# Kernel tuning notes

Measured on AMD Instinct MI355X. Metric: run time of the kernel, lower is better.

Reference implementation:

```python
import jax, jax.numpy as jnp
import numpy as np

T, B, IN, H, L = 512, 64, 512, 512, 2
GATE = 4 * H


def setup_inputs() -> dict:
    key = jax.random.key(0)
    ks = jax.random.split(key, 8)
    s_in = 1.0 / np.sqrt(IN)
    s_h = 1.0 / np.sqrt(H)
    return {
        "x": jax.random.normal(ks[0], (T, B, IN), dtype=jnp.float32),
        # layer 0 params (nn.Linear stores weight as [out, in]; y = x @ W.T + b)
        "Wi0": jax.random.uniform(ks[1], (GATE, IN), jnp.float32, -s_in, s_in),
        "bi0": jax.random.uniform(ks[2], (GATE,), jnp.float32, -s_in, s_in),
        "Wh0": jax.random.uniform(ks[3], (GATE, H), jnp.float32, -s_h, s_h),
        # layer 1 params
        "Wi1": jax.random.uniform(ks[4], (GATE, H), jnp.float32, -s_h, s_h),
        "bi1": jax.random.uniform(ks[5], (GATE,), jnp.float32, -s_h, s_h),
        "Wh1": jax.random.uniform(ks[6], (GATE, H), jnp.float32, -s_h, s_h),
    }


def _run_layer(x_seq, Wi, bi, Wh):
    """Scan the subLSTM cell over time. x_seq: [T, B, in] -> [T, B, H]."""
    Bs = x_seq.shape[1]
    h0 = jnp.zeros((Bs, H), x_seq.dtype)
    c0 = jnp.zeros((Bs, H), x_seq.dtype)

    def cell(carry, x_t):
        h, c = carry
        # all four gates are sigmoid in subLSTM
        g = jax.nn.sigmoid(x_t @ Wi.T + bi + h @ Wh.T)  # [B, 4H]
        in_gate, out_gate, z_t, f_gate = jnp.split(g, 4, axis=-1)
        c_new = c * f_gate + z_t - in_gate          # subtractive combine
        h_new = jax.nn.sigmoid(c_new) - out_gate    # subtractive output
        return (h_new, c_new), h_new

    (_, _), out = jax.lax.scan(cell, (h0, c0), x_seq)
    return out


def reference(x, Wi0, bi0, Wh0, Wi1, bi1, Wh1):
    out = _run_layer(x, Wi0, bi0, Wh0)
    out = _run_layer(out, Wi1, bi1, Wh1)
    return out  # [T, B, H] (batch_first=False, dropout=0)
```

## Files before the change

### kernel.cpp

```cpp
#include <hip/hip_runtime.h>
#include <stdint.h>

#define TSTEPS 512
#define BATCH  64
#define HDIM   512
#define GATE   2048
#define ACTMAT (BATCH * HDIM)
#define SENT   0xFFFFFFFFu
#define NWORK  128

typedef __attribute__((ext_vector_type(8))) _Float16 f16x8;
typedef __attribute__((ext_vector_type(4))) float f32x4;
typedef __attribute__((ext_vector_type(4))) uint32_t u32x4;
typedef __attribute__((ext_vector_type(2))) uint32_t u32x2;

__device__ __forceinline__ unsigned short f2h(float f) {
  union { _Float16 h; unsigned short u; } v;
  v.h = (_Float16)f;
  return v.u;
}
__device__ __forceinline__ float fsigmoid(float x) {
  return 1.0f / (1.0f + __expf(-x));
}


__global__ void init_h(unsigned short* h0, unsigned short* h1) {
  size_t u = (size_t)blockIdx.x * blockDim.x + threadIdx.x;
  u32x4 v;
  if (u < (ACTMAT * 2 / 16)) v = (u32x4){0u, 0u, 0u, 0u};
  else                       v = (u32x4){SENT, SENT, SENT, SENT};
  ((u32x4*)h0)[u] = v;
  ((u32x4*)h1)[u] = v;
}

__global__ void convert_x(const float* __restrict__ x, unsigned short* __restrict__ xh) {
  size_t i = (size_t)(blockIdx.x * blockDim.x + threadIdx.x) * 4;
  float4 v = *(const float4*)(x + i);
  ushort4 o = make_ushort4(f2h(v.x), f2h(v.y), f2h(v.z), f2h(v.w));
  *(ushort4*)(xh + i) = o;
}

__global__ void split_w(const float* __restrict__ Wi, const float* __restrict__ Wh,
                        unsigned short* __restrict__ Wf) {
  int i = blockIdx.x * blockDim.x + threadIdx.x;
  int G = i >> 10, k = i & 1023;
  float w = (k < 512) ? Wi[((size_t)G << 9) + k] : Wh[((size_t)G << 9) + (k - 512)];
  Wf[i] = f2h(w);
}


__global__ __launch_bounds__(128, 1)
void sublstm_persistent(const unsigned short* __restrict__ xh,
                        unsigned short* h0, unsigned short* h1,
                        const unsigned short* __restrict__ Wf0,
                        const unsigned short* __restrict__ Wf1,
                        const float* __restrict__ bi0, const float* __restrict__ bi1,
                        float* __restrict__ out)
{
  __shared__ unsigned short wlds[64][1024];

  const int wg    = blockIdx.x;
  const int tid   = threadIdx.x;
  const int layer = wg >> 6;
  const int wgl   = wg & 63;
  const int s     = wgl & 31;
  const int p     = wgl >> 5;
  const int j0    = s << 4;
  const int b0    = p << 5;
  const int lane  = tid & 63;
  const int wr    = tid >> 6;

  const unsigned short* Wf = layer ? Wf1 : Wf0;
  const float* bi = layer ? bi1 : bi0;

  for (int idx = tid; idx < 8192; idx += 128) {
    int n = idx >> 7;
    int u = idx & 127;
    int G = ((n >> 4) << 9) + j0 + (n & 15);
    const unsigned short* sp = Wf + ((size_t)G << 10) + ((size_t)u << 3);
    *(uint4*)&wlds[n][(u ^ (n & 15)) << 3] = *(const uint4*)sp;
  }
  __syncthreads();

  const int c15 = lane & 15;
  const int g4  = lane >> 4;
  const int sw  = c15;
  const int brow = b0 + (wr << 4) + c15;
  const int jb   = j0 + (g4 << 2);
  const size_t arow = (size_t)brow * HDIM;
  const size_t hoff = arow + jb;

  const float4 bq0 = *(const float4*)&bi[jb];
  const float4 bq1 = *(const float4*)&bi[512 + jb];
  const float4 bq2 = *(const float4*)&bi[1024 + jb];
  const float4 bq3 = *(const float4*)&bi[1536 + jb];

  float cs0 = 0.0f, cs1 = 0.0f, cs2 = 0.0f, cs3 = 0.0f;

#define CONSUME(R, KK, UB) do {                                                        \
    f16x8 a = __builtin_bit_cast(f16x8, (R));                                          \
    int u_ = ((UB) + ((KK) << 2) + g4) ^ sw;                                           \
    f16x8 w0 = *(const f16x8*)&wlds[c15][u_ << 3];                                     \
    f16x8 w1 = *(const f16x8*)&wlds[16 + c15][u_ << 3];                                \
    f16x8 w2 = *(const f16x8*)&wlds[32 + c15][u_ << 3];                                \
    f16x8 w3 = *(const f16x8*)&wlds[48 + c15][u_ << 3];                                \
    acc0 = __builtin_amdgcn_mfma_f32_16x16x32_f16(w0, a, acc0, 0, 0, 0);               \
    acc1 = __builtin_amdgcn_mfma_f32_16x16x32_f16(w1, a, acc1, 0, 0, 0);               \
    acc2 = __builtin_amdgcn_mfma_f32_16x16x32_f16(w2, a, acc2, 0, 0, 0);               \
    acc3 = __builtin_amdgcn_mfma_f32_16x16x32_f16(w3, a, acc3, 0, 0, 0);               \
  } while (0)

#define CONSUME_ALL(P, UB)                                                             \
    CONSUME(P##0, 0, UB);  CONSUME(P##1, 1, UB);  CONSUME(P##2, 2, UB);                \
    CONSUME(P##3, 3, UB);  CONSUME(P##4, 4, UB);  CONSUME(P##5, 5, UB);                \
    CONSUME(P##6, 6, UB);  CONSUME(P##7, 7, UB);  CONSUME(P##8, 8, UB);                \
    CONSUME(P##9, 9, UB);  CONSUME(P##10, 10, UB); CONSUME(P##11, 11, UB);             \
    CONSUME(P##12, 12, UB); CONSUME(P##13, 13, UB); CONSUME(P##14, 14, UB);            \
    CONSUME(P##15, 15, UB)

#define LD1(R, OFFTOK, HP)                                                             \
    asm volatile("global_load_dwordx4 %0, %1, off " OFFTOK " sc0 sc1"                  \
                 : "=v"(R) : "v"(HP) : "memory")

#define ISSUE16(HP, P) do {                                                            \
    LD1(P##0, "", HP);            LD1(P##1, "offset:64", HP);                          \
    LD1(P##2, "offset:128", HP);  LD1(P##3, "offset:192", HP);                         \
    LD1(P##4, "offset:256", HP);  LD1(P##5, "offset:320", HP);                         \
    LD1(P##6, "offset:384", HP);  LD1(P##7, "offset:448", HP);                         \
    LD1(P##8, "offset:512", HP);  LD1(P##9, "offset:576", HP);                         \
    LD1(P##10, "offset:640", HP); LD1(P##11, "offset:704", HP);                        \
    LD1(P##12, "offset:768", HP); LD1(P##13, "offset:832", HP);                        \
    LD1(P##14, "offset:896", HP); LD1(P##15, "offset:960", HP);                        \
  } while (0)

#define BAD1(R) ((R[0] == SENT) | (R[1] == SENT) | (R[2] == SENT) | (R[3] == SENT))

#define VALIDATE(HP, P) do {                                                           \
    for (;;) {                                                                         \
      asm volatile("s_waitcnt vmcnt(0)" ::: "memory");                                 \
      __builtin_amdgcn_sched_barrier(0);                                               \
      int bad_ = BAD1(P##0) | BAD1(P##1) | BAD1(P##2) | BAD1(P##3) |                   \
                 BAD1(P##4) | BAD1(P##5) | BAD1(P##6) | BAD1(P##7) |                   \
                 BAD1(P##8) | BAD1(P##9) | BAD1(P##10) | BAD1(P##11) |                 \
                 BAD1(P##12) | BAD1(P##13) | BAD1(P##14) | BAD1(P##15);                \
      if (!__any(bad_)) break;                                                         \
      ISSUE16(HP, P);                                                                  \
    }                                                                                  \
    __builtin_amdgcn_sched_barrier(0);                                                 \
  } while (0)

#define KHALF_X(AP) do {                                                               \
    const unsigned short* ap_ = (AP) + arow + (g4 << 3);                               \
    _Pragma("unroll")                                                                  \
    for (int kk = 0; kk < 16; ++kk) {                                                  \
      u32x4 rr = *(const u32x4*)(ap_ + (kk << 5));                                     \
      CONSUME(rr, kk, 0);                                                              \
    }                                                                                  \
  } while (0)

#define EPILOGUE(T) do {                                                               \
    unsigned short* hn = (layer ? h1 : h0) + (size_t)((T) + 1) * ACTMAT;               \
    float gi_, go_, gz_, gf_, h0v, h1v, h2v, h3v;                                      \
    gi_ = fsigmoid(acc0[0] + bq0.x); go_ = fsigmoid(acc1[0] + bq1.x);                  \
    gz_ = fsigmoid(acc2[0] + bq2.x); gf_ = fsigmoid(acc3[0] + bq3.x);                  \
    cs0 = cs0 * gf_ + gz_ - gi_;  h0v = fsigmoid(cs0) - go_;                           \
    gi_ = fsigmoid(acc0[1] + bq0.y); go_ = fsigmoid(acc1[1] + bq1.y);                  \
    gz_ = fsigmoid(acc2[1] + bq2.y); gf_ = fsigmoid(acc3[1] + bq3.y);                  \
    cs1 = cs1 * gf_ + gz_ - gi_;  h1v = fsigmoid(cs1) - go_;                           \
    gi_ = fsigmoid(acc0[2] + bq0.z); go_ = fsigmoid(acc1[2] + bq1.z);                  \
    gz_ = fsigmoid(acc2[2] + bq2.z); gf_ = fsigmoid(acc3[2] + bq3.z);                  \
    cs2 = cs2 * gf_ + gz_ - gi_;  h2v = fsigmoid(cs2) - go_;                           \
    gi_ = fsigmoid(acc0[3] + bq0.w); go_ = fsigmoid(acc1[3] + bq1.w);                  \
    gz_ = fsigmoid(acc2[3] + bq2.w); gf_ = fsigmoid(acc3[3] + bq3.w);                  \
    cs3 = cs3 * gf_ + gz_ - gi_;  h3v = fsigmoid(cs3) - go_;                           \
    u32x2 dv;                                                                          \
    dv[0] = (uint32_t)f2h(h0v) | ((uint32_t)f2h(h1v) << 16);                           \
    dv[1] = (uint32_t)f2h(h2v) | ((uint32_t)f2h(h3v) << 16);                           \
    asm volatile("global_store_dwordx2 %0, %1, off sc0 sc1"                            \
                 :: "v"((uint32_t*)(hn + hoff)), "v"(dv) : "memory");                  \
    if (layer) {                                                                       \
      float* outp = out + (size_t)(T) * ACTMAT;                                        \
      *(float4*)(outp + hoff) = make_float4(h0v, h1v, h2v, h3v);                       \
    }                                                                                  \
  } while (0)

  if (layer == 0) {
    for (int t = 0; t < TSTEPS; ++t) {
      f32x4 acc0 = {}, acc1 = {}, acc2 = {}, acc3 = {};
      u32x4 ra0, ra1, ra2, ra3, ra4, ra5, ra6, ra7,
            ra8, ra9, ra10, ra11, ra12, ra13, ra14, ra15;
      const unsigned short* hp = h0 + (size_t)t * ACTMAT + arow + (g4 << 3);
      ISSUE16(hp, ra);
      KHALF_X(xh + (size_t)t * ACTMAT);
      VALIDATE(hp, ra);
      CONSUME_ALL(ra, 64);
      EPILOGUE(t);
    }
  } else {
    for (int t = 0; t < TSTEPS; ++t) {
      f32x4 acc0 = {}, acc1 = {}, acc2 = {}, acc3 = {};
      u32x4 ra0, ra1, ra2, ra3, ra4, ra5, ra6, ra7,
            ra8, ra9, ra10, ra11, ra12, ra13, ra14, ra15;
      u32x4 rb0, rb1, rb2, rb3, rb4, rb5, rb6, rb7,
            rb8, rb9, rb10, rb11, rb12, rb13, rb14, rb15;
      const unsigned short* hpA = h1 + (size_t)t * ACTMAT + arow + (g4 << 3);
      const unsigned short* hpB = h0 + (size_t)(t + 1) * ACTMAT + arow + (g4 << 3);
      ISSUE16(hpA, ra);
      ISSUE16(hpB, rb);
      VALIDATE(hpA, ra);
      CONSUME_ALL(ra, 64);
      VALIDATE(hpB, rb);
      CONSUME_ALL(rb, 0);
      EPILOGUE(t);
    }
  }
#undef CONSUME
#undef CONSUME_ALL
#undef LD1
#undef ISSUE16
#undef BAD1
#undef VALIDATE
#undef KHALF_X
#undef EPILOGUE
}


extern "C" void kernel_launch(void* const* d_in, const int* in_sizes, int n_in,
                              void* d_out, int out_size, void* d_ws, size_t ws_size,
                              hipStream_t stream) {
  (void)in_sizes; (void)n_in; (void)out_size; (void)ws_size;
  const float* x   = (const float*)d_in[0];
  const float* Wi0 = (const float*)d_in[1];
  const float* bi0 = (const float*)d_in[2];
  const float* Wh0 = (const float*)d_in[3];
  const float* Wi1 = (const float*)d_in[4];
  const float* bi1 = (const float*)d_in[5];
  const float* Wh1 = (const float*)d_in[6];
  float* out = (float*)d_out;

  char* ws = (char*)d_ws;
  size_t off = 0;
  auto take = [&](size_t bytes) -> void* {
    void* p = ws + off;
    off += (bytes + 255) & ~(size_t)255;
    return p;
  };
  unsigned short* xh  = (unsigned short*)take((size_t)TSTEPS * ACTMAT * 2);
  unsigned short* h0  = (unsigned short*)take((size_t)(TSTEPS + 1) * ACTMAT * 2);
  unsigned short* h1  = (unsigned short*)take((size_t)(TSTEPS + 1) * ACTMAT * 2);
  unsigned short* Wf0 = (unsigned short*)take((size_t)GATE * 1024 * 2);
  unsigned short* Wf1 = (unsigned short*)take((size_t)GATE * 1024 * 2);

  init_h<<<dim3(8208), dim3(256), 0, stream>>>(h0, h1);
  convert_x<<<dim3(16384), dim3(256), 0, stream>>>(x, xh);
  split_w<<<dim3(8192), dim3(256), 0, stream>>>(Wi0, Wh0, Wf0);
  split_w<<<dim3(8192), dim3(256), 0, stream>>>(Wi1, Wh1, Wf1);
  sublstm_persistent<<<dim3(NWORK), dim3(128), 0, stream>>>(
      xh, h0, h1, Wf0, Wf1, bi0, bi1, out);
}
```

Baseline: 3.869 ms.

## Place recurrent workgroups per XCC so same-layer polling shares L2

The kernel now launches 256 workgroups. Each reads its XCC id and claims a slot through atomic counters. If the first four XCCs each get 32 workgroups, every (layer, batch-half) group is placed on one XCC. Its own-layer h is then written with an extra non-coherent store and polled with L2-cached loads (sc1 only) for the first retries, which avoids round trips to memory. Retries now reload only the chunks still holding the sentinel instead of all 16. The cost is a grid-wide handshake at startup and a dependence on XCC-local L2 coherence. There is a fallback mode if the placement does not work out.

```diff
diff --git a/kernel.cpp b/kernel.cpp
--- a/kernel.cpp
+++ b/kernel.cpp
@@ -7,7 +7,7 @@
 #define GATE   2048
 #define ACTMAT (BATCH * HDIM)
 #define SENT   0xFFFFFFFFu
-#define NWORK  128
+#define NWGTOT 256
 
 typedef __attribute__((ext_vector_type(8))) _Float16 f16x8;
 typedef __attribute__((ext_vector_type(4))) float f32x4;
@@ -24,8 +24,10 @@
 }
 
 
-__global__ void init_h(unsigned short* h0, unsigned short* h1) {
+__global__ void init_h(unsigned short* h0, unsigned short* h1, int* ctrs) {
   size_t u = (size_t)blockIdx.x * blockDim.x + threadIdx.x;
+  if (u < 16)
+    __hip_atomic_store(&ctrs[u], 0, __ATOMIC_RELAXED, __HIP_MEMORY_SCOPE_AGENT);
   u32x4 v;
   if (u < (ACTMAT * 2 / 16)) v = (u32x4){0u, 0u, 0u, 0u};
   else                       v = (u32x4){SENT, SENT, SENT, SENT};
@@ -55,23 +57,64 @@
                         const unsigned short* __restrict__ Wf0,
                         const unsigned short* __restrict__ Wf1,
                         const float* __restrict__ bi0, const float* __restrict__ bi1,
-                        float* __restrict__ out)
+                        float* __restrict__ out, int* ctrs)
 {
   __shared__ unsigned short wlds[64][1024];
 
-  const int wg    = blockIdx.x;
-  const int tid   = threadIdx.x;
-  const int layer = wg >> 6;
-  const int wgl   = wg & 63;
-  const int s     = wgl & 31;
-  const int p     = wgl >> 5;
-  const int j0    = s << 4;
-  const int b0    = p << 5;
-  const int lane  = tid & 63;
-  const int wr    = tid >> 6;
+  const int tid  = threadIdx.x;
+  const int lane = tid & 63;
+  const int wr   = tid >> 6;
+
+  volatile int* roleShare = (volatile int*)&wlds[0][0];
+
+  if (tid == 0) {
+    int xcc;
+    asm volatile("s_getreg_b32 %0, hwreg(HW_REG_XCC_ID)" : "=s"(xcc));
+    xcc &= 7;
+    int slot = atomicAdd(&ctrs[xcc], 1);
+    int g    = atomicAdd(&ctrs[8], 1);
+    atomicAdd(&ctrs[9], 1);
+    if (g == 0) {
+      for (int it = 0; it < (1 << 20); ++it) {
+        if (__hip_atomic_load(&ctrs[9], __ATOMIC_RELAXED, __HIP_MEMORY_SCOPE_AGENT)
+            >= NWGTOT) break;
+        __builtin_amdgcn_s_sleep(8);
+      }
+      int ok = 1;
+      for (int xx = 0; xx < 4; ++xx)
+        if (__hip_atomic_load(&ctrs[xx], __ATOMIC_RELAXED, __HIP_MEMORY_SCOPE_AGENT) < 32)
+          ok = 0;
+      __hip_atomic_store(&ctrs[10], ok ? 1 : 2, __ATOMIC_RELAXED,
+                         __HIP_MEMORY_SCOPE_AGENT);
+    }
+    int mode;
+    while ((mode = __hip_atomic_load(&ctrs[10], __ATOMIC_RELAXED,
+                                     __HIP_MEMORY_SCOPE_AGENT)) == 0)
+      __builtin_amdgcn_s_sleep(2);
+    int layer = -1, p = 0, slice = 0;
+    if (mode == 1) {
+      if (xcc < 4 && slot < 32) { layer = xcc >> 1; p = xcc & 1; slice = slot; }
+    } else {
+      if (g < 128) { layer = (g >> 6) & 1; p = (g >> 5) & 1; slice = g & 31; }
+    }
+    roleShare[0] = mode; roleShare[1] = layer; roleShare[2] = p; roleShare[3] = slice;
+  }
+  __syncthreads();
+  const int mode  = roleShare[0];
+  const int layer = roleShare[1];
+  const int p     = roleShare[2];
+  const int slice = roleShare[3];
+  __syncthreads();
+  if (layer < 0) return;
+  const bool fastm = (mode == 1);
+  const int K1fast = fastm ? 24 : 0;
+
+  const int j0 = slice << 4;
+  const int b0 = p << 5;
 
   const unsigned short* Wf = layer ? Wf1 : Wf0;
   const float* bi = layer ? bi1 : bi0;
+  unsigned short* selfH = layer ? h1 : h0;
 
   for (int idx = tid; idx < 8192; idx += 128) {
     int n = idx >> 7;
@@ -118,33 +161,60 @@
     CONSUME(P##12, 12, UB); CONSUME(P##13, 13, UB); CONSUME(P##14, 14, UB);            \
     CONSUME(P##15, 15, UB)
 
-#define LD1(R, OFFTOK, HP)                                                             \
+#define LD1X(R, OFFTOK, HP)                                                            \
     asm volatile("global_load_dwordx4 %0, %1, off " OFFTOK " sc0 sc1"                  \
                  : "=v"(R) : "v"(HP) : "memory")
-
-#define ISSUE16(HP, P) do {                                                            \
-    LD1(P##0, "", HP);            LD1(P##1, "offset:64", HP);                          \
-    LD1(P##2, "offset:128", HP);  LD1(P##3, "offset:192", HP);                         \
-    LD1(P##4, "offset:256", HP);  LD1(P##5, "offset:320", HP);                         \
-    LD1(P##6, "offset:384", HP);  LD1(P##7, "offset:448", HP);                         \
-    LD1(P##8, "offset:512", HP);  LD1(P##9, "offset:576", HP);                         \
-    LD1(P##10, "offset:640", HP); LD1(P##11, "offset:704", HP);                        \
-    LD1(P##12, "offset:768", HP); LD1(P##13, "offset:832", HP);                        \
-    LD1(P##14, "offset:896", HP); LD1(P##15, "offset:960", HP);                        \
+#define LD1P(R, OFFTOK, HP)                                                            \
+    asm volatile("global_load_dwordx4 %0, %1, off " OFFTOK                             \
+                 : "=v"(R) : "v"(HP) : "memory")
+
+#define ISSUE16X(HP, P) do {                                                           \
+    LD1X(P##0, "", HP);            LD1X(P##1, "offset:64", HP);                        \
+    LD1X(P##2, "offset:128", HP);  LD1X(P##3, "offset:192", HP);                       \
+    LD1X(P##4, "offset:256", HP);  LD1X(P##5, "offset:320", HP);                       \
+    LD1X(P##6, "offset:384", HP);  LD1X(P##7, "offset:448", HP);                       \
+    LD1X(P##8, "offset:512", HP);  LD1X(P##9, "offset:576", HP);                       \
+    LD1X(P##10, "offset:640", HP); LD1X(P##11, "offset:704", HP);                      \
+    LD1X(P##12, "offset:768", HP); LD1X(P##13, "offset:832", HP);                      \
+    LD1X(P##14, "offset:896", HP); LD1X(P##15, "offset:960", HP);                      \
+  } while (0)
+
+#define ISSUE16P(HP, P) do {                                                           \
+    LD1P(P##0, "", HP);            LD1P(P##1, "offset:64", HP);                        \
+    LD1P(P##2, "offset:128", HP);  LD1P(P##3, "offset:192", HP);                       \
+    LD1P(P##4, "offset:256", HP);  LD1P(P##5, "offset:320", HP);                       \
+    LD1P(P##6, "offset:384", HP);  LD1P(P##7, "offset:448", HP);                       \
+    LD1P(P##8, "offset:512", HP);  LD1P(P##9, "offset:576", HP);                       \
+    LD1P(P##10, "offset:640", HP); LD1P(P##11, "offset:704", HP);                      \
+    LD1P(P##12, "offset:768", HP); LD1P(P##13, "offset:832", HP);                      \
+    LD1P(P##14, "offset:896", HP); LD1P(P##15, "offset:960", HP);                      \
   } while (0)
 
 #define BAD1(R) ((R[0] == SENT) | (R[1] == SENT) | (R[2] == SENT) | (R[3] == SENT))
 
-#define VALIDATE(HP, P) do {                                                           \
+#define RET(R, K)                                                                      \
+    if (__any(BAD1(R))) { ++nbad_;                                                     \
+      if (it_ < K1_) {                                                                 \
+        asm volatile("global_load_dwordx4 %0, %1, off sc1"                             \
+                     : "=v"(R) : "v"(hp_ + ((K) << 5)) : "memory");                    \
+      } else {                                                                         \
+        asm volatile("global_load_dwordx4 %0, %1, off sc0 sc1"                         \
+                     : "=v"(R) : "v"(hp_ + ((K) << 5)) : "memory"); } }
+
+#define VALT(P, HP, K1) do {                                                           \
+    const unsigned short* hp_ = (HP);                                                  \
+    const int K1_ = (K1);                                                              \
+    int it_ = 0;                                                                       \
     for (;;) {                                                                         \
       asm volatile("s_waitcnt vmcnt(0)" ::: "memory");                                 \
       __builtin_amdgcn_sched_barrier(0);                                               \
-      int bad_ = BAD1(P##0) | BAD1(P##1) | BAD1(P##2) | BAD1(P##3) |                   \
-                 BAD1(P##4) | BAD1(P##5) | BAD1(P##6) | BAD1(P##7) |                   \
-                 BAD1(P##8) | BAD1(P##9) | BAD1(P##10) | BAD1(P##11) |                 \
-                 BAD1(P##12) | BAD1(P##13) | BAD1(P##14) | BAD1(P##15);                \
-      if (!__any(bad_)) break;                                                         \
-      ISSUE16(HP, P);                                                                  \
+      int nbad_ = 0;                                                                   \
+      RET(P##0, 0)   RET(P##1, 1)   RET(P##2, 2)   RET(P##3, 3)                        \
+      RET(P##4, 4)   RET(P##5, 5)   RET(P##6, 6)   RET(P##7, 7)                        \
+      RET(P##8, 8)   RET(P##9, 9)   RET(P##10, 10) RET(P##11, 11)                      \
+      RET(P##12, 12) RET(P##13, 13) RET(P##14, 14) RET(P##15, 15)                      \
+      if (!nbad_) break;                                                               \
+      ++it_;                                                                           \
     }                                                                                  \
     __builtin_amdgcn_sched_barrier(0);                                                 \
   } while (0)
@@ -159,7 +229,7 @@
   } while (0)
 
 #define EPILOGUE(T) do {                                                               \
-    unsigned short* hn = (layer ? h1 : h0) + (size_t)((T) + 1) * ACTMAT;               \
+    unsigned short* hn = selfH + (size_t)((T) + 1) * ACTMAT;                           \
     float gi_, go_, gz_, gf_, h0v, h1v, h2v, h3v;                                      \
     gi_ = fsigmoid(acc0[0] + bq0.x); go_ = fsigmoid(acc1[0] + bq1.x);                  \
     gz_ = fsigmoid(acc2[0] + bq2.x); gf_ = fsigmoid(acc3[0] + bq3.x);                  \
@@ -176,7 +246,10 @@
     u32x2 dv;                                                                          \
     dv[0] = (uint32_t)f2h(h0v) | ((uint32_t)f2h(h1v) << 16);                           \
     dv[1] = (uint32_t)f2h(h2v) | ((uint32_t)f2h(h3v) << 16);                           \
-    asm volatile("global_store_dwordx2 %0, %1, off sc0 sc1"                            \
+    if (fastm)                                                                         \
+      asm volatile("global_store_dwordx2 %0, %1, off"                  \
+                   :: "v"((uint32_t*)(hn + hoff)), "v"(dv) : "memory");                \
+    asm volatile("global_store_dwordx2 %0, %1, off sc0 sc1"             \
                  :: "v"((uint32_t*)(hn + hoff)), "v"(dv) : "memory");                  \
     if (layer) {                                                                       \
       float* outp = out + (size_t)(T) * ACTMAT;                                        \
@@ -190,9 +263,9 @@
       u32x4 ra0, ra1, ra2, ra3, ra4, ra5, ra6, ra7,
             ra8, ra9, ra10, ra11, ra12, ra13, ra14, ra15;
       const unsigned short* hp = h0 + (size_t)t * ACTMAT + arow + (g4 << 3);
-      ISSUE16(hp, ra);
+      if (fastm) ISSUE16P(hp, ra); else ISSUE16X(hp, ra);
       KHALF_X(xh + (size_t)t * ACTMAT);
-      VALIDATE(hp, ra);
+      VALT(ra, hp, K1fast);
       CONSUME_ALL(ra, 64);
       EPILOGUE(t);
     }
@@ -205,21 +278,24 @@
             rb8, rb9, rb10, rb11, rb12, rb13, rb14, rb15;
       const unsigned short* hpA = h1 + (size_t)t * ACTMAT + arow + (g4 << 3);
       const unsigned short* hpB = h0 + (size_t)(t + 1) * ACTMAT + arow + (g4 << 3);
-      ISSUE16(hpA, ra);
-      ISSUE16(hpB, rb);
-      VALIDATE(hpA, ra);
+      ISSUE16X(hpB, rb);
+      if (fastm) ISSUE16P(hpA, ra); else ISSUE16X(hpA, ra);
+      VALT(ra, hpA, K1fast);
       CONSUME_ALL(ra, 64);
-      VALIDATE(hpB, rb);
+      VALT(rb, hpB, 0);
       CONSUME_ALL(rb, 0);
       EPILOGUE(t);
     }
   }
 #undef CONSUME
 #undef CONSUME_ALL
-#undef LD1
-#undef ISSUE16
+#undef LD1X
+#undef LD1P
+#undef ISSUE16X
+#undef ISSUE16P
 #undef BAD1
-#undef VALIDATE
+#undef RET
+#undef VALT
 #undef KHALF_X
 #undef EPILOGUE
 }
@@ -250,11 +326,12 @@
   unsigned short* h1  = (unsigned short*)take((size_t)(TSTEPS + 1) * ACTMAT * 2);
   unsigned short* Wf0 = (unsigned short*)take((size_t)GATE * 1024 * 2);
   unsigned short* Wf1 = (unsigned short*)take((size_t)GATE * 1024 * 2);
-
-  init_h<<<dim3(8208), dim3(256), 0, stream>>>(h0, h1);
+  int* ctrs           = (int*)take(64);
+
+  init_h<<<dim3(8208), dim3(256), 0, stream>>>(h0, h1, ctrs);
   convert_x<<<dim3(16384), dim3(256), 0, stream>>>(x, xh);
   split_w<<<dim3(8192), dim3(256), 0, stream>>>(Wi0, Wh0, Wf0);
   split_w<<<dim3(8192), dim3(256), 0, stream>>>(Wi1, Wh1, Wf1);
-  sublstm_persistent<<<dim3(NWORK), dim3(128), 0, stream>>>(
-      xh, h0, h1, Wf0, Wf1, bi0, bi1, out);
-}
+  sublstm_persistent<<<dim3(NWGTOT), dim3(128), 0, stream>>>(
+      xh, h0, h1, Wf0, Wf1, bi0, bi1, out, ctrs);
+}
```

Result: slower. 4.971 ms (+28.5%).
